# Performance work log

Hardware: AMD Instinct MI355X
Metric: run time of the kernel (lower is better)

Reference implementation:

```python
import jax, jax.numpy as jnp
import numpy as np
import math

EMBED_DIM = 512
NUM_HEADS = 8
HEAD_DIM = EMBED_DIM // NUM_HEADS
B, S = 4, 2048


def setup_inputs() -> dict:
    key = jax.random.key(0)
    ks = jax.random.split(key, 12)
    d = EMBED_DIM
    # Xavier-uniform bound for square linear layers
    bound = math.sqrt(6.0 / (d + d))
    def lin_w(k):
        return jax.random.uniform(k, (d, d), jnp.float32, -bound, bound)
    return {
        "x": jax.random.normal(ks[0], (B, S, d), jnp.float32),
        "mask": jax.random.randint(ks[1], (B, S), 0, 2) == 1,  # True = masked out
        "wq": lin_w(ks[2]), "bq": jnp.zeros((d,), jnp.float32),
        "wk": lin_w(ks[3]), "bk": jnp.zeros((d,), jnp.float32),
        "wv": lin_w(ks[4]), "bv": jnp.zeros((d,), jnp.float32),
        "wo": lin_w(ks[5]), "bo": jnp.zeros((d,), jnp.float32),
        "ln_gamma": jnp.ones((d,), jnp.float32),
        "ln_beta": jnp.zeros((d,), jnp.float32),
        "temperature": jnp.full((1,), 1.0 / math.sqrt(HEAD_DIM), jnp.float32),
    }


def _layer_norm(x, gamma, beta, eps=1e-6):
    mu = jnp.mean(x, axis=-1, keepdims=True)
    var = jnp.var(x, axis=-1, keepdims=True)
    return (x - mu) * jax.lax.rsqrt(var + eps) * gamma + beta


def reference(x, mask, wq, bq, wk, bk, wv, bv, wo, bo, ln_gamma, ln_beta, temperature):
    Bv, Sv, d = x.shape
    H, hd = NUM_HEADS, HEAD_DIM
    # torch nn.Linear: y = x @ W.T + b (W is [out, in])
    def proj(w, b):
        return (jnp.einsum("bsd,ed->bse", x, w) + b).reshape(Bv, Sv, H, hd).transpose(0, 2, 1, 3)
    q = proj(wq, bq)  # [B, H, S, hd]
    k = proj(wk, bk)
    v = proj(wv, bv)
    scores = jnp.einsum("bhqd,bhkd->bhqk", q, k) * temperature[0]  # [B,H,S,S]
    scores = jnp.where(mask[:, None, None, :], jnp.float32(-1e9), scores)
    attn = jax.nn.softmax(scores, axis=-1)  # dropout is identity in eval
    out = jnp.einsum("bhqk,bhkd->bhqd", attn, v)
    out = out.transpose(0, 2, 1, 3).reshape(Bv, Sv, d)
    out = jnp.einsum("bsd,ed->bse", out, wo) + bo
    return _layer_norm(out + x, ln_gamma, ln_beta)
```

## Files before the change

kernel.cpp:

```cpp
#include <hip/hip_runtime.h>
#include <hip/hip_bf16.h>
#include <stdint.h>

#define B_ 4
#define S_ 2048
#define D_ 512
#define H_ 8
#define HD_ 64
#define M_ (B_*S_)

typedef __bf16 bf16x8 __attribute__((ext_vector_type(8)));
typedef float f32x4 __attribute__((ext_vector_type(4)));
typedef float f32x16 __attribute__((ext_vector_type(16)));

__device__ __forceinline__ unsigned short f2b(float f) {
  union { float f; unsigned u; } v; v.f = f;
  unsigned r = v.u + 0x7fff + ((v.u >> 16) & 1);
  return (unsigned short)(r >> 16);
}

__device__ __forceinline__ float b2f(unsigned short u) {
  union { unsigned u; float f; } v; v.u = (unsigned)u << 16;
  return v.f;
}

__device__ __forceinline__ float exp2_hw(float x) {
  return __builtin_amdgcn_exp2f(x);
}

__device__ __forceinline__ unsigned cvtpk_bf16(float lo, float hi) {
  unsigned r;
  asm("v_cvt_pk_bf16_f32 %0, %1, %2" : "=v"(r) : "v"(lo), "v"(hi));
  return r;
}

__device__ __forceinline__ void plswap(unsigned &a, unsigned &b) {
  asm volatile("v_permlane32_swap_b32 %0, %1" : "+v"(a), "+v"(b));
}

__device__ __forceinline__ void gload16(const void* g, void* lds) {
  __builtin_amdgcn_global_load_lds(
      (const __attribute__((address_space(1))) unsigned int*)g,
      (__attribute__((address_space(3))) unsigned int*)lds, 16, 0, 0);
}

#define XN4 (M_ * D_ / 4)
#define WN4 (D_ * D_ / 4)
__global__ __launch_bounds__(256) void cvt_all_kernel(const float* __restrict__ x,
    const float* __restrict__ wq, const float* __restrict__ wk,
    const float* __restrict__ wv, const float* __restrict__ wo,
    unsigned short* __restrict__ xb, unsigned short* __restrict__ wqb,
    unsigned short* __restrict__ wkb, unsigned short* __restrict__ wvb,
    unsigned short* __restrict__ wob) {
  int i = blockIdx.x * blockDim.x + threadIdx.x;
  const float* src; unsigned short* dst; int off;
  if (i < XN4) { src = x; dst = xb; off = i; }
  else {
    int j = i - XN4;
    int sel = j / WN4; off = j - sel * WN4;
    src = (sel == 0) ? wq : (sel == 1) ? wk : (sel == 2) ? wv : wo;
    dst = (sel == 0) ? wqb : (sel == 1) ? wkb : (sel == 2) ? wvb : wob;
  }
  float4 v = ((const float4*)src)[off];
  ushort4 o;
  o.x = f2b(v.x); o.y = f2b(v.y); o.z = f2b(v.z); o.w = f2b(v.w);
  ((ushort4*)dst)[off] = o;
}

__global__ __launch_bounds__(64) void rank_kernel(const int* __restrict__ mask,
    int* __restrict__ idx, int* __restrict__ rank, int* __restrict__ nkbuf) {
  int b = blockIdx.x, lane = threadIdx.x;
  const int* mb = mask + (size_t)b * S_;
  int base = 0;
  for (int c = 0; c < 32; ++c) {
    int s = c * 64 + lane;
    int m = mb[s];
    unsigned long long keep = __ballot(m == 0);
    int my = base + __popcll(keep & ((1ull << lane) - 1ull));
    if (m == 0) idx[(size_t)b * S_ + my] = s;
    rank[(size_t)b * S_ + s] = (m == 0) ? my : -1;
    base += __popcll(keep);
  }
  if (lane == 0) nkbuf[b] = base;
}

__global__ __launch_bounds__(256) void compact_kernel(
    const unsigned short* __restrict__ Vtb, const int* __restrict__ idx,
    const int* __restrict__ nkbuf, unsigned short* __restrict__ Vtc) {
  int bh = blockIdx.y, b = bh >> 3;
  int nk = nkbuf[b];
  const int* ib = idx + (size_t)b * S_;
  int tid = threadIdx.x;
  int d = blockIdx.x;
  const unsigned short* src = &Vtb[((size_t)bh * HD_ + d) * S_];
  unsigned short* dst = &Vtc[((size_t)bh * HD_ + d) * S_];
  int j0 = tid * 8;
  if (j0 < nk) {
    unsigned short tmp[8];
    #pragma unroll
    for (int c = 0; c < 8; ++c) {
      int j = j0 + c;
      tmp[c] = (j < nk) ? src[ib[j]] : (unsigned short)0;
    }
    *(uint4*)&dst[j0] = *(uint4*)tmp;
  }
}

__device__ __forceinline__ void gemm_core_db(const unsigned short* __restrict__ A,
                                             const unsigned short* __restrict__ W,
                                             int m0, int n0, f32x4 (&acc)[4][4],
                                             unsigned short (&As)[2][128 * 64],
                                             unsigned short (&Bs)[2][128 * 64]) {
  int tid = threadIdx.x;
  int w = tid >> 6, lane = tid & 63;
  int l15 = lane & 15, g = lane >> 4;
  int wr = w >> 1, wc = w & 1;
  #define STAGE_G(buf, k0_) do {                                               \
    _Pragma("unroll")                                                          \
    for (int i = 0; i < 4; ++i) {                                              \
      int l = i * 256 + w * 64 + lane;                                         \
      int row = l >> 3, seg = l & 7;                                           \
      int sseg = seg ^ (row & 7);                                              \
      gload16(A + (size_t)(m0 + row) * D_ + (k0_) + sseg * 8,                  \
              (char*)As[buf] + (size_t)(i * 256 + w * 64) * 16);               \
      gload16(W + (size_t)(n0 + row) * D_ + (k0_) + sseg * 8,                  \
              (char*)Bs[buf] + (size_t)(i * 256 + w * 64) * 16);               \
    }                                                                          \
  } while (0)
  STAGE_G(0, 0);
  __syncthreads();
  for (int ks = 0; ks < 8; ++ks) {
    int cur = ks & 1;
    if (ks < 7) STAGE_G(cur ^ 1, (ks + 1) * 64);
    #pragma unroll
    for (int kk = 0; kk < 2; ++kk) {
      int sw = ((kk * 4 + g) ^ (l15 & 7)) * 8;
      bf16x8 af[4], bfr[4];
      #pragma unroll
      for (int t = 0; t < 4; ++t) {
        af[t]  = *(const bf16x8*)&As[cur][(wr * 64 + t * 16 + l15) * 64 + sw];
        bfr[t] = *(const bf16x8*)&Bs[cur][(wc * 64 + t * 16 + l15) * 64 + sw];
      }
      #pragma unroll
      for (int mi = 0; mi < 4; ++mi)
        #pragma unroll
        for (int ni = 0; ni < 4; ++ni)
          acc[mi][ni] = __builtin_amdgcn_mfma_f32_16x16x32_bf16(af[mi], bfr[ni], acc[mi][ni], 0, 0, 0);
    }
    __syncthreads();
  }
  #undef STAGE_G
}

__global__ __launch_bounds__(256) void gemm_qkv(const unsigned short* __restrict__ xb,
    const unsigned short* __restrict__ wqb, const unsigned short* __restrict__ wkb,
    const unsigned short* __restrict__ wvb,
    const float* __restrict__ bq, const float* __restrict__ bk, const float* __restrict__ bv,
    const float* __restrict__ tptr, const int* __restrict__ rank,
    unsigned short* __restrict__ Qb, unsigned short* __restrict__ Kc, unsigned short* __restrict__ Vtb) {
  __shared__ unsigned short As[2][128 * 64], Bs[2][128 * 64];
  int z = blockIdx.z;
  const unsigned short* W = (z == 0) ? wqb : ((z == 1) ? wkb : wvb);
  const float* bias = (z == 0) ? bq : ((z == 1) ? bk : bv);
  float scale = (z == 0) ? tptr[0] * 1.44269504088896340736f : 1.0f;
  int m0 = blockIdx.x * 128, n0 = blockIdx.y * 128;
  f32x4 zero4 = {0.f, 0.f, 0.f, 0.f};
  f32x4 acc[4][4];
  #pragma unroll
  for (int mi = 0; mi < 4; ++mi)
    #pragma unroll
    for (int ni = 0; ni < 4; ++ni) acc[mi][ni] = zero4;
  gemm_core_db(xb, W, m0, n0, acc, As, Bs);
  int tid = threadIdx.x;
  int w = tid >> 6, lane = tid & 63, l15 = lane & 15, g = lane >> 4;
  int wr = w >> 1, wc = w & 1;
  if (z == 2) {
    unsigned short* T = &As[0][0];
    #pragma unroll
    for (int mi = 0; mi < 4; ++mi)
      #pragma unroll
      for (int ni = 0; ni < 4; ++ni) {
        int el = wc * 64 + ni * 16 + l15;
        float bb = bias[n0 + el];
        int sx = (el & 15) << 3;
        #pragma unroll
        for (int r = 0; r < 4; ++r) {
          int s = wr * 64 + mi * 16 + g * 4 + r;
          T[el * 128 + (s ^ sx)] = f2b(acc[mi][ni][r] + bb);
        }
      }
    __syncthreads();
    int el = tid >> 1, hf = tid & 1;
    int eg = n0 + el, h = eg >> 6, dd = eg & 63;
    int bI = m0 >> 11, sbase = (m0 & 2047) + hf * 64;
    unsigned short* dst = &Vtb[((size_t)(bI * H_ + h) * HD_ + dd) * S_ + sbase];
    const unsigned short* srcR = &T[el * 128];
    int j = el & 15;
    #pragma unroll
    for (int c = 0; c < 8; ++c) {
      int cc = (hf * 8 + c) ^ j;
      uint4 v = *(const uint4*)&srcR[cc * 8];
      *(uint4*)&dst[c * 8] = v;
    }
  } else if (z == 1) {
    #pragma unroll
    for (int mi = 0; mi < 4; ++mi)
      #pragma unroll
      for (int ni = 0; ni < 4; ++ni) {
        int e = n0 + wc * 64 + ni * 16 + l15;
        float bb = bias[e];
        int h = e >> 6, dd = e & 63;
        #pragma unroll
        for (int r = 0; r < 4; ++r) {
          int m = m0 + wr * 64 + mi * 16 + g * 4 + r;
          int b = m >> 11, s = m & 2047;
          int jj = rank[(size_t)b * S_ + s];
          if (jj >= 0) {
            unsigned short u = f2b(acc[mi][ni][r] + bb);
            Kc[((size_t)(b * H_ + h) * S_ + jj) * HD_ + dd] = u;
          }
        }
      }
  } else {
    #pragma unroll
    for (int mi = 0; mi < 4; ++mi)
      #pragma unroll
      for (int ni = 0; ni < 4; ++ni) {
        int e = n0 + wc * 64 + ni * 16 + l15;
        float bb = bias[e];
        int h = e >> 6, dd = e & 63;
        #pragma unroll
        for (int r = 0; r < 4; ++r) {
          int m = m0 + wr * 64 + mi * 16 + g * 4 + r;
          int b = m >> 11, s = m & 2047;
          unsigned short u = f2b((acc[mi][ni][r] + bb) * scale);
          Qb[((size_t)(b * H_ + h) * S_ + s) * HD_ + dd] = u;
        }
      }
  }
}

__global__ __launch_bounds__(256) void gemm_proj(const unsigned short* __restrict__ AOb,
    const unsigned short* __restrict__ wob, const float* __restrict__ bo,
    unsigned short* __restrict__ Pfb) {
  __shared__ unsigned short As[2][128 * 64], Bs[2][128 * 64];
  int m0 = blockIdx.x * 128, n0 = blockIdx.y * 128;
  f32x4 zero4 = {0.f, 0.f, 0.f, 0.f};
  f32x4 acc[4][4];
  #pragma unroll
  for (int mi = 0; mi < 4; ++mi)
    #pragma unroll
    for (int ni = 0; ni < 4; ++ni) acc[mi][ni] = zero4;
  gemm_core_db(AOb, wob, m0, n0, acc, As, Bs);
  int tid = threadIdx.x;
  int w = tid >> 6, lane = tid & 63, l15 = lane & 15, g = lane >> 4;
  int wr = w >> 1, wc = w & 1;
  #pragma unroll
  for (int mi = 0; mi < 4; ++mi)
    #pragma unroll
    for (int ni = 0; ni < 4; ++ni) {
      int e = n0 + wc * 64 + ni * 16 + l15;
      float bb = bo[e];
      #pragma unroll
      for (int r = 0; r < 4; ++r) {
        int m = m0 + wr * 64 + mi * 16 + g * 4 + r;
        Pfb[(size_t)m * D_ + e] = f2b(acc[mi][ni][r] + bb);
      }
    }
}

__global__ __launch_bounds__(256, 2) void attn_kernel(const unsigned short* __restrict__ Qb,
    const unsigned short* __restrict__ Kc, const unsigned short* __restrict__ Vtc,
    const int* __restrict__ nkbuf, unsigned short* __restrict__ AOb) {
  __shared__ unsigned short Ks[3][64 * 64], Vs[3][64 * 64];
  __shared__ uint4 mlds[32][4][2];
  int bid = blockIdx.y * gridDim.x + blockIdx.x;
  int xcd = bid & 7, jj = bid >> 3;
  int bh = xcd * 4 + (jj >> 4);
  int qblk = jj & 15;
  int b = bh >> 3, h = bh & 7;
  int tid = threadIdx.x, w = tid >> 6, lane = tid & 63;
  int l31 = lane & 31, hi = lane >> 5;
  int q0w = qblk * 128 + w * 32;
  const unsigned short* Qbase = Qb + (size_t)bh * S_ * HD_;
  int nk = nkbuf[b];
  int nt = (nk + 63) >> 6;

  bf16x8 qf[4];
  #pragma unroll
  for (int kk = 0; kk < 4; ++kk)
    qf[kk] = *(const bf16x8*)&Qbase[(size_t)(q0w + l31) * HD_ + kk * 16 + hi * 8];

  bf16x8 ones;
  #pragma unroll
  for (int c = 0; c < 8; ++c) ones[c] = (__bf16)1.0f;

  f32x16 out[2], lacc, zc;
  #pragma unroll
  for (int i = 0; i < 16; ++i) { out[0][i] = 0.f; out[1][i] = 0.f; lacc[i] = 0.f; zc[i] = 0.f; }

  f32x16 stA[2], stB[2];

  #define STAGE_KV(buf, kb_) do {                                              \
    _Pragma("unroll")                                                          \
    for (int i = 0; i < 2; ++i) {                                              \
      int l = i * 256 + w * 64 + lane;                                         \
      int row = l >> 3, seg = l & 7;                                           \
      int sseg = seg ^ (row & 7);                                              \
      gload16(Kc + ((size_t)bh * S_ + (kb_) + row) * HD_ + sseg * 8,           \
              (char*)Ks[buf] + (size_t)(i * 256 + w * 64) * 16);               \
      gload16(Vtc + ((size_t)bh * HD_ + row) * S_ + (kb_) + sseg * 8,          \
              (char*)Vs[buf] + (size_t)(i * 256 + w * 64) * 16);               \
    }                                                                          \
  } while (0)

  #define QKT_TILE(KSBUF, ST) do {                                             \
    __builtin_amdgcn_s_setprio(1);                                             \
    const unsigned short* kbase_ = Ks[KSBUF];                                  \
    _Pragma("unroll")                                                          \
    for (int kk = 0; kk < 4; ++kk) {                                           \
      int sw = ((2 * kk + hi) ^ (l31 & 7)) * 8;                                \
      bf16x8 ka0 = *(const bf16x8*)&kbase_[l31 * 64 + sw];                     \
      bf16x8 ka1 = *(const bf16x8*)&kbase_[(32 + l31) * 64 + sw];              \
      ST[0] = __builtin_amdgcn_mfma_f32_32x32x16_bf16(ka0, qf[kk], kk ? ST[0] : zc, 0, 0, 0); \
      ST[1] = __builtin_amdgcn_mfma_f32_32x32x16_bf16(ka1, qf[kk], kk ? ST[1] : zc, 0, 0, 0); \
    }                                                                          \
    __builtin_amdgcn_s_setprio(0);                                             \
  } while (0)

  #define TILE_BODY(T, STC, STN, bPV, bQK, bST) do {                           \
    __syncthreads();                                                           \
    if ((T) + 2 < nt) STAGE_KV(bST, ((T) + 2) * 64);                           \
    if ((T) + 1 < nt) QKT_TILE(bQK, STN);                                      \
    _Pragma("unroll")                                                          \
    for (int ktile = 0; ktile < 2; ++ktile)                                    \
      _Pragma("unroll")                                                        \
      for (int reg = 0; reg < 16; ++reg)                                       \
        STC[ktile][reg] = exp2_hw(STC[ktile][reg]);                            \
    __builtin_amdgcn_s_setprio(1);                                             \
    const unsigned short* vbase_ = Vs[bPV];                                    \
    _Pragma("unroll")                                                          \
    for (int kp = 0; kp < 4; ++kp) {                                           \
      const int kt8 = kp >> 1;                                                 \
      const int ro = 8 * (kp & 1);                                             \
      uint4 mw = mlds[(T)][kp][hi];                                            \
      unsigned Xa = cvtpk_bf16(STC[kt8][ro + 0], STC[kt8][ro + 1]);            \
      unsigned Ya = cvtpk_bf16(STC[kt8][ro + 4], STC[kt8][ro + 5]);            \
      unsigned Xb = cvtpk_bf16(STC[kt8][ro + 2], STC[kt8][ro + 3]);            \
      unsigned Yb = cvtpk_bf16(STC[kt8][ro + 6], STC[kt8][ro + 7]);            \
      plswap(Xa, Ya);                                                          \
      plswap(Xb, Yb);                                                          \
      union { unsigned u[4]; bf16x8 v; } pu;                                   \
      pu.u[0] = Xa & mw.x; pu.u[1] = Xb & mw.y;                                \
      pu.u[2] = Ya & mw.z; pu.u[3] = Yb & mw.w;                                \
      bf16x8 pa = pu.v;                                                        \
      _Pragma("unroll")                                                        \
      for (int dn = 0; dn < 2; ++dn) {                                         \
        int row = dn * 32 + l31;                                               \
        bf16x8 vb = *(const bf16x8*)&vbase_[row * 64 + ((2 * kp + hi) ^ (row & 7)) * 8]; \
        out[dn] = __builtin_amdgcn_mfma_f32_32x32x16_bf16(pa, vb, out[dn], 0, 0, 0); \
      }                                                                        \
      lacc = __builtin_amdgcn_mfma_f32_32x32x16_bf16(pa, ones, lacc, 0, 0, 0); \
    }                                                                          \
    __builtin_amdgcn_s_setprio(0);                                             \
  } while (0)

  STAGE_KV(0, 0);
  {
    int t = tid;
    int tile = t >> 3, kp = (t >> 1) & 3, hh = t & 1;
    int j0 = tile * 64 + kp * 16 + hh * 8;
    uint4 mw;
    mw.x = ((j0 + 0 < nk) ? 0x0000FFFFu : 0u) | ((j0 + 1 < nk) ? 0xFFFF0000u : 0u);
    mw.y = ((j0 + 2 < nk) ? 0x0000FFFFu : 0u) | ((j0 + 3 < nk) ? 0xFFFF0000u : 0u);
    mw.z = ((j0 + 4 < nk) ? 0x0000FFFFu : 0u) | ((j0 + 5 < nk) ? 0xFFFF0000u : 0u);
    mw.w = ((j0 + 6 < nk) ? 0x0000FFFFu : 0u) | ((j0 + 7 < nk) ? 0xFFFF0000u : 0u);
    mlds[tile][kp][hh] = mw;
  }
  __syncthreads();
  if (nt > 1) STAGE_KV(1, 64);
  QKT_TILE(0, stA);

  int t = 0;
  for (; t + 1 < nt; t += 2) {
    TILE_BODY(t, stA, stB, t % 3, (t + 1) % 3, (t + 2) % 3);
    TILE_BODY(t + 1, stB, stA, (t + 1) % 3, (t + 2) % 3, t % 3);
  }
  if (t < nt) TILE_BODY(t, stA, stB, t % 3, (t + 1) % 3, (t + 2) % 3);

  #pragma unroll
  for (int reg = 0; reg < 16; ++reg) {
    float inv = 1.f / lacc[reg];
    int q = q0w + (reg & 3) + 8 * (reg >> 2) + 4 * hi;
    #pragma unroll
    for (int dn = 0; dn < 2; ++dn)
      AOb[((size_t)b * S_ + q) * D_ + h * HD_ + dn * 32 + l31] = f2b(out[dn][reg] * inv);
  }
  #undef TILE_BODY
  #undef QKT_TILE
  #undef STAGE_KV
}

__global__ __launch_bounds__(256) void ln_kernel(const unsigned short* __restrict__ Pfb,
    const float* __restrict__ x, const float* __restrict__ gamma,
    const float* __restrict__ beta, float* __restrict__ out) {
  int row = blockIdx.x * 4 + (threadIdx.x >> 6);
  int lane = threadIdx.x & 63;
  const unsigned short* pr = Pfb + (size_t)row * D_;
  const float* xr = x + (size_t)row * D_;
  ushort4 p0 = *(const ushort4*)(pr + lane * 8);
  ushort4 p1 = *(const ushort4*)(pr + lane * 8 + 4);
  float4 b0 = *(const float4*)(xr + lane * 8);
  float4 b1 = *(const float4*)(xr + lane * 8 + 4);
  float y[8] = {b2f(p0.x) + b0.x, b2f(p0.y) + b0.y, b2f(p0.z) + b0.z, b2f(p0.w) + b0.w,
                b2f(p1.x) + b1.x, b2f(p1.y) + b1.y, b2f(p1.z) + b1.z, b2f(p1.w) + b1.w};
  float s = 0.f, s2 = 0.f;
  #pragma unroll
  for (int i = 0; i < 8; ++i) { s += y[i]; s2 += y[i] * y[i]; }
  #pragma unroll
  for (int d = 1; d < 64; d <<= 1) { s += __shfl_xor(s, d); s2 += __shfl_xor(s2, d); }
  float mu = s * (1.f / 512.f);
  float var = s2 * (1.f / 512.f) - mu * mu;
  float inv = rsqrtf(fmaxf(var, 0.f) + 1e-6f);
  float4 g0 = *(const float4*)(gamma + lane * 8);
  float4 g1 = *(const float4*)(gamma + lane * 8 + 4);
  float4 e0 = *(const float4*)(beta + lane * 8);
  float4 e1 = *(const float4*)(beta + lane * 8 + 4);
  float* orow = out + (size_t)row * D_;
  float4 o0 = {(y[0] - mu) * inv * g0.x + e0.x, (y[1] - mu) * inv * g0.y + e0.y,
               (y[2] - mu) * inv * g0.z + e0.z, (y[3] - mu) * inv * g0.w + e0.w};
  float4 o1 = {(y[4] - mu) * inv * g1.x + e1.x, (y[5] - mu) * inv * g1.y + e1.y,
               (y[6] - mu) * inv * g1.z + e1.z, (y[7] - mu) * inv * g1.w + e1.w};
  *(float4*)(orow + lane * 8) = o0;
  *(float4*)(orow + lane * 8 + 4) = o1;
}

extern "C" void kernel_launch(void* const* d_in, const int* in_sizes, int n_in,
                              void* d_out, int out_size, void* d_ws, size_t ws_size,
                              hipStream_t stream) {
  const float* x = (const float*)d_in[0];
  const int* mask = (const int*)d_in[1];
  const float* wq = (const float*)d_in[2];
  const float* bq = (const float*)d_in[3];
  const float* wk = (const float*)d_in[4];
  const float* bk = (const float*)d_in[5];
  const float* wv = (const float*)d_in[6];
  const float* bv = (const float*)d_in[7];
  const float* wo = (const float*)d_in[8];
  const float* bo = (const float*)d_in[9];
  const float* gamma = (const float*)d_in[10];
  const float* beta = (const float*)d_in[11];
  const float* temp = (const float*)d_in[12];
  float* out = (float*)d_out;
  char* ws = (char*)d_ws;
  const size_t MB = (size_t)1 << 20;
  unsigned short* xb  = (unsigned short*)(ws);
  unsigned short* wqb = (unsigned short*)(ws + 8 * MB);
  unsigned short* wkb = (unsigned short*)(ws + 8 * MB + 512 * 1024);
  unsigned short* wvb = (unsigned short*)(ws + 9 * MB);
  unsigned short* wob = (unsigned short*)(ws + 9 * MB + 512 * 1024);
  unsigned short* Qb  = (unsigned short*)(ws + 10 * MB);
  unsigned short* Pfb = (unsigned short*)(ws + 18 * MB);
  unsigned short* Vtb = (unsigned short*)(ws + 26 * MB);
  unsigned short* AOb = (unsigned short*)(ws + 34 * MB);
  unsigned short* Kc  = (unsigned short*)(ws + 42 * MB);
  unsigned short* Vtc = (unsigned short*)(ws + 50 * MB);
  int*            idx = (int*)(ws + 58 * MB);
  int*            rnk = (int*)(ws + 58 * MB + 64 * 1024);
  int*            nkb = (int*)(ws + 58 * MB + 128 * 1024);

  cvt_all_kernel<<<(XN4 + 4 * WN4 + 255) / 256, 256, 0, stream>>>(
      x, wq, wk, wv, wo, xb, wqb, wkb, wvb, wob);
  rank_kernel<<<4, 64, 0, stream>>>(mask, idx, rnk, nkb);
  gemm_qkv<<<dim3(64, 4, 3), 256, 0, stream>>>(xb, wqb, wkb, wvb, bq, bk, bv, temp, rnk, Qb, Kc, Vtb);
  compact_kernel<<<dim3(64, 32), 256, 0, stream>>>(Vtb, idx, nkb, Vtc);
  attn_kernel<<<dim3(16, 32), 256, 0, stream>>>(Qb, Kc, Vtc, nkb, AOb);
  gemm_proj<<<dim3(64, 4), 256, 0, stream>>>(AOb, wob, bo, Pfb);
  ln_kernel<<<2048, 256, 0, stream>>>(Pfb, x, gamma, beta, out);
}
```

Before: 99.11 us.

## Fuse Q/K/V projections into one kernel reusing a resident x tile

The QKV GEMM now runs one block per 64-row by 128-column tile, loads the full 64x512 slice of x into LDS once, and loops over the Q, K and V weights. Only weight tiles are double-buffered, and the next weight's first tile is prefetched across the z boundary. This removes the threefold re-read of x from the old grid-z split and halves the per-block M tile. The trade-off is larger LDS use (96 KB), which may cut occupancy, and fewer accumulators per wave.

```diff
diff --git a/kernel.cpp b/kernel.cpp
--- a/kernel.cpp
+++ b/kernel.cpp
@@ -158,86 +158,139 @@
     const float* __restrict__ bq, const float* __restrict__ bk, const float* __restrict__ bv,
     const float* __restrict__ tptr, const int* __restrict__ rank,
     unsigned short* __restrict__ Qb, unsigned short* __restrict__ Kc, unsigned short* __restrict__ Vtb) {
-  __shared__ unsigned short As[2][128 * 64], Bs[2][128 * 64];
-  int z = blockIdx.z;
-  const unsigned short* W = (z == 0) ? wqb : ((z == 1) ? wkb : wvb);
-  const float* bias = (z == 0) ? bq : ((z == 1) ? bk : bv);
-  float scale = (z == 0) ? tptr[0] * 1.44269504088896340736f : 1.0f;
-  int m0 = blockIdx.x * 128, n0 = blockIdx.y * 128;
-  f32x4 zero4 = {0.f, 0.f, 0.f, 0.f};
-  f32x4 acc[4][4];
-  #pragma unroll
-  for (int mi = 0; mi < 4; ++mi)
-    #pragma unroll
-    for (int ni = 0; ni < 4; ++ni) acc[mi][ni] = zero4;
-  gemm_core_db(xb, W, m0, n0, acc, As, Bs);
+  __shared__ unsigned short Alds[8][64 * 64];
+  __shared__ unsigned short Blds[2][128 * 64];
   int tid = threadIdx.x;
-  int w = tid >> 6, lane = tid & 63, l15 = lane & 15, g = lane >> 4;
-  int wr = w >> 1, wc = w & 1;
-  if (z == 2) {
-    unsigned short* T = &As[0][0];
+  int w = tid >> 6, lane = tid & 63;
+  int l15 = lane & 15, g = lane >> 4;
+  int m0 = blockIdx.x * 64, n0 = blockIdx.y * 128;
+  const unsigned short* Ws[3] = {wqb, wkb, wvb};
+  const float* biases[3] = {bq, bk, bv};
+  float qscale = tptr[0] * 1.44269504088896340736f;
+
+  #define STAGE_A(ck) do {                                                     \
+    _Pragma("unroll")                                                          \
+    for (int i = 0; i < 2; ++i) {                                              \
+      int l = i * 256 + w * 64 + lane;                                         \
+      int row = l >> 3, seg = l & 7;                                           \
+      int sseg = seg ^ (row & 7);                                              \
+      gload16(xb + (size_t)(m0 + row) * D_ + (ck) * 64 + sseg * 8,             \
+              (char*)&Alds[ck][0] + (size_t)(i * 256 + w * 64) * 16);          \
+    }                                                                          \
+  } while (0)
+  #define STAGE_B(buf, Wp, k0_) do {                                           \
+    _Pragma("unroll")                                                          \
+    for (int i = 0; i < 4; ++i) {                                              \
+      int l = i * 256 + w * 64 + lane;                                         \
+      int row = l >> 3, seg = l & 7;                                           \
+      int sseg = seg ^ (row & 7);                                              \
+      gload16((Wp) + (size_t)(n0 + row) * D_ + (k0_) + sseg * 8,               \
+              (char*)&Blds[buf][0] + (size_t)(i * 256 + w * 64) * 16);         \
+    }                                                                          \
+  } while (0)
+
+  #pragma unroll
+  for (int ck = 0; ck < 8; ++ck) STAGE_A(ck);
+  STAGE_B(0, Ws[0], 0);
+  __syncthreads();
+
+  #pragma unroll
+  for (int z = 0; z < 3; ++z) {
+    f32x4 zero4 = {0.f, 0.f, 0.f, 0.f};
+    f32x4 acc[4][2];
     #pragma unroll
     for (int mi = 0; mi < 4; ++mi)
       #pragma unroll
-      for (int ni = 0; ni < 4; ++ni) {
-        int el = wc * 64 + ni * 16 + l15;
-        float bb = bias[n0 + el];
-        int sx = (el & 15) << 3;
-        #pragma unroll
-        for (int r = 0; r < 4; ++r) {
-          int s = wr * 64 + mi * 16 + g * 4 + r;
-          T[el * 128 + (s ^ sx)] = f2b(acc[mi][ni][r] + bb);
-        }
+      for (int ni = 0; ni < 2; ++ni) acc[mi][ni] = zero4;
+    for (int ks = 0; ks < 8; ++ks) {
+      int cur = ks & 1;
+      if (ks < 7) STAGE_B(cur ^ 1, Ws[z], (ks + 1) * 64);
+      else if (z < 2) STAGE_B(cur ^ 1, Ws[z + 1], 0);
+      #pragma unroll
+      for (int kk = 0; kk < 2; ++kk) {
+        int sw = ((kk * 4 + g) ^ (l15 & 7)) * 8;
+        bf16x8 af[4], bfr[2];
+        #pragma unroll
+        for (int t = 0; t < 4; ++t)
+          af[t] = *(const bf16x8*)&Alds[ks][(t * 16 + l15) * 64 + sw];
+        #pragma unroll
+        for (int ni = 0; ni < 2; ++ni)
+          bfr[ni] = *(const bf16x8*)&Blds[cur][(w * 32 + ni * 16 + l15) * 64 + sw];
+        #pragma unroll
+        for (int mi = 0; mi < 4; ++mi)
+          #pragma unroll
+          for (int ni = 0; ni < 2; ++ni)
+            acc[mi][ni] = __builtin_amdgcn_mfma_f32_16x16x32_bf16(af[mi], bfr[ni], acc[mi][ni], 0, 0, 0);
       }
-    __syncthreads();
-    int el = tid >> 1, hf = tid & 1;
-    int eg = n0 + el, h = eg >> 6, dd = eg & 63;
-    int bI = m0 >> 11, sbase = (m0 & 2047) + hf * 64;
-    unsigned short* dst = &Vtb[((size_t)(bI * H_ + h) * HD_ + dd) * S_ + sbase];
-    const unsigned short* srcR = &T[el * 128];
-    int j = el & 15;
-    #pragma unroll
-    for (int c = 0; c < 8; ++c) {
-      int cc = (hf * 8 + c) ^ j;
-      uint4 v = *(const uint4*)&srcR[cc * 8];
-      *(uint4*)&dst[c * 8] = v;
+      __syncthreads();
     }
-  } else if (z == 1) {
-    #pragma unroll
-    for (int mi = 0; mi < 4; ++mi)
-      #pragma unroll
-      for (int ni = 0; ni < 4; ++ni) {
-        int e = n0 + wc * 64 + ni * 16 + l15;
-        float bb = bias[e];
-        int h = e >> 6, dd = e & 63;
-        #pragma unroll
-        for (int r = 0; r < 4; ++r) {
-          int m = m0 + wr * 64 + mi * 16 + g * 4 + r;
-          int b = m >> 11, s = m & 2047;
-          int jj = rank[(size_t)b * S_ + s];
-          if (jj >= 0) {
-            unsigned short u = f2b(acc[mi][ni][r] + bb);
-            Kc[((size_t)(b * H_ + h) * S_ + jj) * HD_ + dd] = u;
+    if (z == 2) {
+      unsigned short* T = &Alds[0][0];
+      #pragma unroll
+      for (int mi = 0; mi < 4; ++mi)
+        #pragma unroll
+        for (int ni = 0; ni < 2; ++ni) {
+          int el = w * 32 + ni * 16 + l15;
+          float bb = biases[2][n0 + el];
+          int sx = (el & 7) << 3;
+          #pragma unroll
+          for (int r = 0; r < 4; ++r) {
+            int s = mi * 16 + g * 4 + r;
+            T[el * 64 + (s ^ sx)] = f2b(acc[mi][ni][r] + bb);
           }
         }
+      __syncthreads();
+      int el = tid >> 1, hf = tid & 1;
+      int eg = n0 + el, h = eg >> 6, dd = eg & 63;
+      int bI = m0 >> 11, sbase = (m0 & 2047) + hf * 32;
+      unsigned short* dst = &Vtb[((size_t)(bI * H_ + h) * HD_ + dd) * S_ + sbase];
+      const unsigned short* srcR = &T[el * 64];
+      int jx = el & 7;
+      #pragma unroll
+      for (int c = 0; c < 4; ++c) {
+        int cc = (hf * 4 + c) ^ jx;
+        uint4 v = *(const uint4*)&srcR[cc * 8];
+        *(uint4*)&dst[c * 8] = v;
       }
-  } else {
-    #pragma unroll
-    for (int mi = 0; mi < 4; ++mi)
-      #pragma unroll
-      for (int ni = 0; ni < 4; ++ni) {
-        int e = n0 + wc * 64 + ni * 16 + l15;
-        float bb = bias[e];
-        int h = e >> 6, dd = e & 63;
-        #pragma unroll
-        for (int r = 0; r < 4; ++r) {
-          int m = m0 + wr * 64 + mi * 16 + g * 4 + r;
-          int b = m >> 11, s = m & 2047;
-          unsigned short u = f2b((acc[mi][ni][r] + bb) * scale);
-          Qb[((size_t)(b * H_ + h) * S_ + s) * HD_ + dd] = u;
+    } else if (z == 1) {
+      #pragma unroll
+      for (int mi = 0; mi < 4; ++mi)
+        #pragma unroll
+        for (int ni = 0; ni < 2; ++ni) {
+          int e = n0 + w * 32 + ni * 16 + l15;
+          float bb = biases[1][e];
+          int h = e >> 6, dd = e & 63;
+          #pragma unroll
+          for (int r = 0; r < 4; ++r) {
+            int m = m0 + mi * 16 + g * 4 + r;
+            int b = m >> 11, s = m & 2047;
+            int jj = rank[(size_t)b * S_ + s];
+            if (jj >= 0) {
+              unsigned short u = f2b(acc[mi][ni][r] + bb);
+              Kc[((size_t)(b * H_ + h) * S_ + jj) * HD_ + dd] = u;
+            }
+          }
         }
-      }
-  }
+    } else {
+      #pragma unroll
+      for (int mi = 0; mi < 4; ++mi)
+        #pragma unroll
+        for (int ni = 0; ni < 2; ++ni) {
+          int e = n0 + w * 32 + ni * 16 + l15;
+          float bb = biases[0][e];
+          int h = e >> 6, dd = e & 63;
+          #pragma unroll
+          for (int r = 0; r < 4; ++r) {
+            int m = m0 + mi * 16 + g * 4 + r;
+            int b = m >> 11, s = m & 2047;
+            unsigned short u = f2b((acc[mi][ni][r] + bb) * qscale);
+            Qb[((size_t)(b * H_ + h) * S_ + s) * HD_ + dd] = u;
+          }
+        }
+    }
+  }
+  #undef STAGE_A
+  #undef STAGE_B
 }
 
 __global__ __launch_bounds__(256) void gemm_proj(const unsigned short* __restrict__ AOb,
@@ -472,7 +525,7 @@
   cvt_all_kernel<<<(XN4 + 4 * WN4 + 255) / 256, 256, 0, stream>>>(
       x, wq, wk, wv, wo, xb, wqb, wkb, wvb, wob);
   rank_kernel<<<4, 64, 0, stream>>>(mask, idx, rnk, nkb);
-  gemm_qkv<<<dim3(64, 4, 3), 256, 0, stream>>>(xb, wqb, wkb, wvb, bq, bk, bv, temp, rnk, Qb, Kc, Vtb);
+  gemm_qkv<<<dim3(128, 4), 256, 0, stream>>>(xb, wqb, wkb, wvb, bq, bk, bv, temp, rnk, Qb, Kc, Vtb);
   compact_kernel<<<dim3(64, 32), 256, 0, stream>>>(Vtb, idx, nkb, Vtc);
   attn_kernel<<<dim3(16, 32), 256, 0, stream>>>(Qb, Kc, Vtc, nkb, AOb);
   gemm_proj<<<dim3(64, 4), 256, 0, stream>>>(AOb, wob, bo, Pfb);
```

Measured after the change: 116.0 us. 1.17x slower.
